# Optimization experiments

Measured on AMD Instinct MI355X. Metric: run time of the kernel, lower is better.

The kernel has to match this reference:

```python
import jax, jax.numpy as jnp
import numpy as np
from jax.ops import segment_sum, segment_max

N, E, G = 20000, 100000, 16
TILE, EMB, HID, OUT, FEAT, HEADS = 32, 128, 256, 512, 512, 8
SLOPE = 0.2


def setup_inputs() -> dict:
    key = jax.random.key(0)
    ks = jax.random.split(key, 20)
    def gn(k, shape, fan_in):
        return jax.random.normal(k, shape, jnp.float32) * (1.0 / np.sqrt(fan_in))
    return {
        "x": jax.random.normal(ks[0], (N, TILE), jnp.float32),
        "edge_index": jax.random.randint(ks[1], (2, E), 0, N, jnp.int32),
        "batch": jnp.sort(jax.random.randint(ks[2], (N,), 0, G, jnp.int32)),
        "W0": gn(ks[3], (TILE, EMB), TILE), "b0": jnp.zeros((EMB,), jnp.float32),
        "W1": gn(ks[4], (EMB, HEADS * HID), EMB),
        "a1s": gn(ks[5], (HEADS, HID), HID), "a1d": gn(ks[6], (HEADS, HID), HID),
        "b1": jnp.zeros((HEADS * HID,), jnp.float32),
        "W2": gn(ks[7], (HEADS * HID, HEADS * HID), HEADS * HID),
        "a2s": gn(ks[8], (HEADS, HID), HID), "a2d": gn(ks[9], (HEADS, HID), HID),
        "b2": jnp.zeros((HEADS * HID,), jnp.float32),
        "W3": gn(ks[10], (HEADS * HID, OUT), HEADS * HID),
        "a3s": gn(ks[11], (1, OUT), OUT), "a3d": gn(ks[12], (1, OUT), OUT),
        "b3": jnp.zeros((OUT,), jnp.float32),
        "Wf": gn(ks[13], (OUT, FEAT), OUT), "bf": jnp.zeros((FEAT,), jnp.float32),
    }


def gat_conv(x, src, dst, W, a_s, a_d, b, heads, ch, n):
    # PyG GATConv: linear, per-edge additive attention, segment softmax over dst, scatter-add
    h = (x @ W).reshape(n, heads, ch)                       # [N,H,C]
    e_src = jnp.einsum("nhc,hc->nh", h, a_s)                 # [N,H]
    e_dst = jnp.einsum("nhc,hc->nh", h, a_d)
    e = jax.nn.leaky_relu(e_src[src] + e_dst[dst], SLOPE)    # [E,H]
    m = segment_max(e, dst, num_segments=n)                  # [N,H]
    m = jax.lax.stop_gradient(jnp.where(jnp.isfinite(m), m, 0.0))
    ex = jnp.exp(e - m[dst])
    den = segment_sum(ex, dst, num_segments=n)
    alpha = ex / (den[dst] + 1e-16)                          # [E,H]
    out = segment_sum(h[src] * alpha[..., None], dst, num_segments=n)  # [N,H,C]
    return out.reshape(n, heads * ch) + b


def reference(x, edge_index, batch, W0, b0, W1, a1s, a1d, b1, W2, a2s, a2d, b2,
              W3, a3s, a3d, b3, Wf, bf):
    loop = jnp.arange(N, dtype=edge_index.dtype)             # PyG adds self-loops by default
    src = jnp.concatenate([edge_index[0], loop])
    dst = jnp.concatenate([edge_index[1], loop])
    h = jax.nn.leaky_relu(x @ W0 + b0, SLOPE)
    h = jax.nn.leaky_relu(gat_conv(h, src, dst, W1, a1s, a1d, b1, HEADS, HID, N), SLOPE)
    h = jax.nn.leaky_relu(gat_conv(h, src, dst, W2, a2s, a2d, b2, HEADS, HID, N), SLOPE)
    h = jax.nn.leaky_relu(gat_conv(h, src, dst, W3, a3s, a3d, b3, 1, OUT, N), SLOPE)
    sums = segment_sum(h, batch, num_segments=G)             # global_mean_pool
    cnt = segment_sum(jnp.ones((N,), h.dtype), batch, num_segments=G)
    mean = sums / jnp.maximum(cnt, 1.0)[:, None]
    return jax.nn.leaky_relu(mean @ Wf + bf, SLOPE)
```

## Files before the change

### kernel.cpp

```cpp
#include <hip/hip_runtime.h>
#include <hip/hip_bf16.h>

#define N_NODES 20000
#define N_EDGES 100000
#define ET (N_EDGES + N_NODES)
#define G_GRAPHS 16
#define SLOPE 0.2f

using short8  = __attribute__((ext_vector_type(8))) short;
using floatx4 = __attribute__((ext_vector_type(4))) float;

__device__ __forceinline__ float lrelu(float x) { return x > 0.f ? x : SLOPE * x; }

__device__ __forceinline__ float b2f(unsigned short u) {
    union { unsigned int i; float f; } v; v.i = ((unsigned int)u) << 16; return v.f;
}
__device__ __forceinline__ unsigned short f2b(float f) {
    union { float f; unsigned int i; } v; v.f = f;
    unsigned int i = v.i;
    return (unsigned short)((i + 0x7fffu + ((i >> 16) & 1u)) >> 16);
}

__device__ __forceinline__ void gld16(const void* g, void* l) {
    __builtin_amdgcn_global_load_lds((const __attribute__((address_space(1))) void*)g,
                                     (__attribute__((address_space(3))) void*)l, 16, 0, 0);
}

__device__ int dev_lower_bound(const int* a, int n, int key) {
    int lo = 0, hi = n;
    while (lo < hi) { int mid = (lo + hi) >> 1; if (a[mid] < key) lo = mid + 1; else hi = mid; }
    return lo;
}

__global__ void zero_kernel(int* __restrict__ p, int n) {
    int i = blockIdx.x * blockDim.x + threadIdx.x;
    if (i < n) p[i] = 0;
}

__global__ void count_kernel(const int* __restrict__ ei, int* __restrict__ counts) {
    int e = blockIdx.x * blockDim.x + threadIdx.x;
    if (e >= ET) return;
    int dst = (e < N_EDGES) ? ei[N_EDGES + e] : (e - N_EDGES);
    atomicAdd(&counts[dst], 1);
}

__global__ void scan_kernel(const int* __restrict__ counts, int* __restrict__ row_ptr) {
    __shared__ int sums[256];
    int t = threadIdx.x;
    const int CH = (N_NODES + 255) / 256;
    int base = t * CH;
    int s = 0;
    for (int i = 0; i < CH; i++) { int idx = base + i; if (idx < N_NODES) s += counts[idx]; }
    sums[t] = s;
    __syncthreads();
    for (int off = 1; off < 256; off <<= 1) {
        int v = (t >= off) ? sums[t - off] : 0;
        __syncthreads();
        sums[t] += v;
        __syncthreads();
    }
    int run = (t == 0) ? 0 : sums[t - 1];
    for (int i = 0; i < CH; i++) {
        int idx = base + i;
        if (idx < N_NODES) { row_ptr[idx] = run; run += counts[idx]; }
    }
    if (t == 255) row_ptr[N_NODES] = run;
}

__global__ void fill_kernel(const int* __restrict__ ei, const int* __restrict__ row_ptr,
                            int* __restrict__ fill_cnt, int* __restrict__ col) {
    int e = blockIdx.x * blockDim.x + threadIdx.x;
    if (e >= ET) return;
    int src, dst;
    if (e < N_EDGES) { src = ei[e]; dst = ei[N_EDGES + e]; }
    else             { src = dst = e - N_EDGES; }
    int pos = atomicAdd(&fill_cnt[dst], 1);
    col[row_ptr[dst] + pos] = src;
}

__global__ void transpose_kernel(const float* __restrict__ W, unsigned short* __restrict__ Wt,
                                 int K, int N) {
    __shared__ float tile[32][33];
    int bn = blockIdx.x * 32, bk = blockIdx.y * 32;
    int tx = threadIdx.x & 31, ty = threadIdx.x >> 5;
#pragma unroll
    for (int p = 0; p < 32; p += 8)
        tile[ty + p][tx] = W[(size_t)(bk + ty + p) * N + bn + tx];
    __syncthreads();
#pragma unroll
    for (int p = 0; p < 32; p += 8)
        Wt[(size_t)(bn + ty + p) * K + bk + tx] = f2b(tile[tx][ty + p]);
}

__global__ void gemm0_kernel(const float* __restrict__ x, const float* __restrict__ W0,
                             const float* __restrict__ b0, unsigned short* __restrict__ h0) {
    __shared__ float xr[32];
    int n = blockIdx.x, t = threadIdx.x;
    if (t < 32) xr[t] = x[n * 32 + t];
    __syncthreads();
    float acc = 0.f;
#pragma unroll
    for (int k = 0; k < 32; k++) acc += xr[k] * W0[k * 128 + t];
    h0[(size_t)n * 128 + t] = f2b(lrelu(acc + b0[t]));
}

__global__ __launch_bounds__(256) void gemm_mfma(const unsigned short* __restrict__ A,
                                                 const unsigned short* __restrict__ Bt,
                                                 unsigned short* __restrict__ C,
                                                 int M, int N, int K) {
    __shared__ __align__(16) unsigned short As[128][32];
    __shared__ __align__(16) unsigned short Bs[128][32];
    int t = threadIdx.x;
    int w = t >> 6, l = t & 63;
    int r0 = blockIdx.y * 128, c0 = blockIdx.x * 128;
    int wr = (w >> 1) * 64, wc = (w & 1) * 64;
    int lrow = l >> 2;
    int gcb  = (l & 3) ^ ((l >> 3) & 3);
    int m16 = l & 15, qb = l >> 4;
    int sw  = (m16 >> 1) & 3;
    int roff = ((qb ^ sw) * 8);
    floatx4 acc[4][4] = {};

    for (int k0 = 0; k0 < K; k0 += 32) {
        __syncthreads();
#pragma unroll
        for (int q = 0; q < 2; q++) {
            int row = w * 32 + q * 16 + lrow;
            int ga = min(r0 + row, M - 1);
            gld16(A + (size_t)ga * K + k0 + gcb * 8, &As[w * 32 + q * 16][0]);
            gld16(Bt + (size_t)(c0 + row) * K + k0 + gcb * 8, &Bs[w * 32 + q * 16][0]);
        }
        __syncthreads();
        short8 af[4], bfr[4];
#pragma unroll
        for (int i = 0; i < 4; i++) af[i] = *(const short8*)&As[wr + i * 16 + m16][roff];
#pragma unroll
        for (int j = 0; j < 4; j++) bfr[j] = *(const short8*)&Bs[wc + j * 16 + m16][roff];
#pragma unroll
        for (int i = 0; i < 4; i++)
#pragma unroll
            for (int j = 0; j < 4; j++)
                acc[i][j] = __builtin_amdgcn_mfma_f32_16x16x32_bf16(bfr[j], af[i], acc[i][j], 0, 0, 0);
    }
    int quad = l >> 4;
#pragma unroll
    for (int i = 0; i < 4; i++) {
        int r = r0 + wr + i * 16 + m16;
        if (r < M) {
#pragma unroll
            for (int j = 0; j < 4; j++) {
                int c = c0 + wc + j * 16 + quad * 4;
                ushort4 o = make_ushort4(f2b(acc[i][j][0]), f2b(acc[i][j][1]),
                                         f2b(acc[i][j][2]), f2b(acc[i][j][3]));
                *(ushort4*)&C[(size_t)r * N + c] = o;
            }
        }
    }
}

__global__ void att8_kernel(const unsigned short* __restrict__ h, const float* __restrict__ a_s,
                            const float* __restrict__ a_d, float* __restrict__ es,
                            float* __restrict__ ed) {
    int n = blockIdx.x, t = threadIdx.x;
    int hd = t >> 5, l = t & 31;
    const unsigned short* hr = h + (size_t)n * 2048 + hd * 256 + l * 8;
    const float* as_ = a_s + hd * 256 + l * 8;
    const float* ad_ = a_d + hd * 256 + l * 8;
    uint4 u = *(const uint4*)hr;
    float v[8] = { b2f((unsigned short)(u.x & 0xffff)), b2f((unsigned short)(u.x >> 16)),
                   b2f((unsigned short)(u.y & 0xffff)), b2f((unsigned short)(u.y >> 16)),
                   b2f((unsigned short)(u.z & 0xffff)), b2f((unsigned short)(u.z >> 16)),
                   b2f((unsigned short)(u.w & 0xffff)), b2f((unsigned short)(u.w >> 16)) };
    float s1 = 0.f, s2 = 0.f;
#pragma unroll
    for (int j = 0; j < 8; j++) { s1 += v[j] * as_[j]; s2 += v[j] * ad_[j]; }
    for (int m = 16; m >= 1; m >>= 1) { s1 += __shfl_xor(s1, m); s2 += __shfl_xor(s2, m); }
    if (l == 0) { es[n * 8 + hd] = s1; ed[n * 8 + hd] = s2; }
}

__global__ void att1_kernel(const unsigned short* __restrict__ h, const float* __restrict__ a_s,
                            const float* __restrict__ a_d, float* __restrict__ es,
                            float* __restrict__ ed) {
    int n = blockIdx.x, l = threadIdx.x;
    const unsigned short* hr = h + (size_t)n * 512 + l * 8;
    const float* as_ = a_s + l * 8;
    const float* ad_ = a_d + l * 8;
    uint4 u = *(const uint4*)hr;
    float v[8] = { b2f((unsigned short)(u.x & 0xffff)), b2f((unsigned short)(u.x >> 16)),
                   b2f((unsigned short)(u.y & 0xffff)), b2f((unsigned short)(u.y >> 16)),
                   b2f((unsigned short)(u.z & 0xffff)), b2f((unsigned short)(u.z >> 16)),
                   b2f((unsigned short)(u.w & 0xffff)), b2f((unsigned short)(u.w >> 16)) };
    float s1 = 0.f, s2 = 0.f;
#pragma unroll
    for (int j = 0; j < 8; j++) { s1 += v[j] * as_[j]; s2 += v[j] * ad_[j]; }
    for (int m = 32; m >= 1; m >>= 1) { s1 += __shfl_xor(s1, m); s2 += __shfl_xor(s2, m); }
    if (l == 0) { es[n] = s1; ed[n] = s2; }
}

template <int H, int C>
__global__ __launch_bounds__(256) void agg_fused(const unsigned short* __restrict__ hmid,
                                                 const float* __restrict__ es,
                                                 const float* __restrict__ ed,
                                                 const int* __restrict__ row_ptr,
                                                 const int* __restrict__ col,
                                                 const float* __restrict__ bias,
                                                 unsigned short* __restrict__ out) {
    constexpr int HC = H * C;
    constexpr int PT = HC / 256;
    int v = blockIdx.x, t = threadIdx.x;
    int rs = row_ptr[v], deg = row_ptr[v + 1] - rs;
    int j0 = t * PT;
    int hd = j0 / C;
    float edv = ed[v * H + hd];
    float acc[PT] = {};
    float den = 0.f;
    int sN = (deg > 0) ? col[rs] : 0;
    for (int e = 0; e < deg; e++) {
        int s = sN;
        if (e + 1 < deg) sN = col[rs + e + 1];
        float a = __expf(lrelu(es[s * H + hd] + edv));
        den += a;
        const unsigned short* hr = hmid + (size_t)s * HC + j0;
        if constexpr (PT == 8) {
            uint4 u = *(const uint4*)hr;
            acc[0] += a * b2f((unsigned short)(u.x & 0xffff));
            acc[1] += a * b2f((unsigned short)(u.x >> 16));
            acc[2] += a * b2f((unsigned short)(u.y & 0xffff));
            acc[3] += a * b2f((unsigned short)(u.y >> 16));
            acc[4] += a * b2f((unsigned short)(u.z & 0xffff));
            acc[5] += a * b2f((unsigned short)(u.z >> 16));
            acc[6] += a * b2f((unsigned short)(u.w & 0xffff));
            acc[7] += a * b2f((unsigned short)(u.w >> 16));
        } else {
            unsigned int u = *(const unsigned int*)hr;
            acc[0] += a * b2f((unsigned short)(u & 0xffff));
            acc[1] += a * b2f((unsigned short)(u >> 16));
        }
    }
    float inv = 1.f / (den + 1e-16f);
    unsigned short o[PT];
#pragma unroll
    for (int i = 0; i < PT; i++) o[i] = f2b(lrelu(acc[i] * inv + bias[j0 + i]));
    if constexpr (PT == 8) {
        *(uint4*)&out[(size_t)v * HC + j0] = *(const uint4*)o;
    } else {
        *(unsigned int*)&out[(size_t)v * HC + j0] = *(const unsigned int*)o;
    }
}

__global__ void pool_kernel(const unsigned short* __restrict__ h3, const int* __restrict__ batch,
                            float* __restrict__ msum) {
    int b0 = blockIdx.x * 128, t = threadIdx.x;
    int nend = min(b0 + 128, N_NODES);
    int curg = batch[b0];
    float s0 = 0.f, s1 = 0.f;
    for (int n = b0; n < nend; n++) {
        int g = batch[n];
        if (g != curg) {
            atomicAdd(&msum[curg * 512 + t * 2], s0);
            atomicAdd(&msum[curg * 512 + t * 2 + 1], s1);
            s0 = s1 = 0.f; curg = g;
        }
        unsigned int u = *(const unsigned int*)&h3[(size_t)n * 512 + t * 2];
        s0 += b2f((unsigned short)(u & 0xffff));
        s1 += b2f((unsigned short)(u >> 16));
    }
    atomicAdd(&msum[curg * 512 + t * 2], s0);
    atomicAdd(&msum[curg * 512 + t * 2 + 1], s1);
}

__global__ void final_kernel(const float* __restrict__ msum, const int* __restrict__ batch,
                             const float* __restrict__ Wf, const float* __restrict__ bf,
                             float* __restrict__ out) {
    int g = blockIdx.x, t = threadIdx.x;
    __shared__ float mr[512];
    __shared__ float sinv;
    if (t == 0) {
        int st = dev_lower_bound(batch, N_NODES, g);
        int en = dev_lower_bound(batch, N_NODES, g + 1);
        sinv = 1.f / fmaxf((float)(en - st), 1.f);
    }
    __syncthreads();
    for (int c = t; c < 512; c += 256) mr[c] = msum[g * 512 + c] * sinv;
    __syncthreads();
    for (int j = t; j < 512; j += 256) {
        float s = 0.f;
        for (int k = 0; k < 512; k++) s += mr[k] * Wf[k * 512 + j];
        out[g * 512 + j] = lrelu(s + bf[j]);
    }
}

extern "C" void kernel_launch(void* const* d_in, const int* in_sizes, int n_in,
                              void* d_out, int out_size, void* d_ws, size_t ws_size,
                              hipStream_t stream) {
    const float* x   = (const float*)d_in[0];
    const int*   ei  = (const int*)d_in[1];
    const int*   bat = (const int*)d_in[2];
    const float* W0  = (const float*)d_in[3];
    const float* b0  = (const float*)d_in[4];
    const float* W1  = (const float*)d_in[5];
    const float* a1s = (const float*)d_in[6];
    const float* a1d = (const float*)d_in[7];
    const float* b1  = (const float*)d_in[8];
    const float* W2  = (const float*)d_in[9];
    const float* a2s = (const float*)d_in[10];
    const float* a2d = (const float*)d_in[11];
    const float* b2  = (const float*)d_in[12];
    const float* W3  = (const float*)d_in[13];
    const float* a3s = (const float*)d_in[14];
    const float* a3d = (const float*)d_in[15];
    const float* b3  = (const float*)d_in[16];
    const float* Wf  = (const float*)d_in[17];
    const float* bf  = (const float*)d_in[18];
    float* out = (float*)d_out;

    char* p = (char*)d_ws;
    unsigned short* bufA = (unsigned short*)p; p += (size_t)N_NODES * 2048 * 2;
    unsigned short* bufB = (unsigned short*)p; p += (size_t)N_NODES * 2048 * 2;
    unsigned short* h0   = (unsigned short*)p; p += (size_t)N_NODES * 128 * 2;
    unsigned short* W1t  = (unsigned short*)p; p += (size_t)2048 * 128 * 2;
    unsigned short* W2t  = (unsigned short*)p; p += (size_t)2048 * 2048 * 2;
    unsigned short* W3t  = (unsigned short*)p; p += (size_t)512 * 2048 * 2;
    float* es   = (float*)p; p += (size_t)N_NODES * 8 * 4;
    float* ed   = (float*)p; p += (size_t)N_NODES * 8 * 4;
    float* msum = (float*)p; p += 16 * 512 * 4;
    int* counts  = (int*)p; p += (size_t)N_NODES * 4;
    int* row_ptr = (int*)p; p += (size_t)(N_NODES + 1) * 4;
    int* col     = (int*)p; p += (size_t)ET * 4;

    zero_kernel<<<(N_NODES + 255) / 256, 256, 0, stream>>>(counts, N_NODES);
    count_kernel<<<(ET + 255) / 256, 256, 0, stream>>>(ei, counts);
    scan_kernel<<<1, 256, 0, stream>>>(counts, row_ptr);
    zero_kernel<<<(N_NODES + 255) / 256, 256, 0, stream>>>(counts, N_NODES);
    fill_kernel<<<(ET + 255) / 256, 256, 0, stream>>>(ei, row_ptr, counts, col);

    transpose_kernel<<<dim3(2048 / 32, 128 / 32), 256, 0, stream>>>(W1, W1t, 128, 2048);
    transpose_kernel<<<dim3(2048 / 32, 2048 / 32), 256, 0, stream>>>(W2, W2t, 2048, 2048);
    transpose_kernel<<<dim3(512 / 32, 2048 / 32), 256, 0, stream>>>(W3, W3t, 2048, 512);

    gemm0_kernel<<<N_NODES, 128, 0, stream>>>(x, W0, b0, h0);

    dim3 g12(2048 / 128, (N_NODES + 127) / 128);
    dim3 g3(512 / 128, (N_NODES + 127) / 128);

    gemm_mfma<<<g12, 256, 0, stream>>>(h0, W1t, bufB, N_NODES, 2048, 128);
    att8_kernel<<<N_NODES, 256, 0, stream>>>(bufB, a1s, a1d, es, ed);
    agg_fused<8, 256><<<N_NODES, 256, 0, stream>>>(bufB, es, ed, row_ptr, col, b1, bufA);

    gemm_mfma<<<g12, 256, 0, stream>>>(bufA, W2t, bufB, N_NODES, 2048, 2048);
    att8_kernel<<<N_NODES, 256, 0, stream>>>(bufB, a2s, a2d, es, ed);
    agg_fused<8, 256><<<N_NODES, 256, 0, stream>>>(bufB, es, ed, row_ptr, col, b2, bufA);

    gemm_mfma<<<g3, 256, 0, stream>>>(bufA, W3t, bufB, N_NODES, 512, 2048);
    att1_kernel<<<N_NODES, 64, 0, stream>>>(bufB, a3s, a3d, es, ed);
    agg_fused<1, 512><<<N_NODES, 256, 0, stream>>>(bufB, es, ed, row_ptr, col, b3, bufA);

    zero_kernel<<<(16 * 512 + 255) / 256, 256, 0, stream>>>((int*)msum, 16 * 512);
    pool_kernel<<<(N_NODES + 127) / 128, 256, 0, stream>>>(bufA, bat, msum);
    final_kernel<<<G_GRAPHS, 256, 0, stream>>>(msum, bat, Wf, bf, out);
}
```

Measured before the change: 827.7 us.

## Fuse attention-score dot products into GEMM epilogue and use wave-per-node aggregation

The attention logits (h·a_src, h·a_dst) are now computed in the MFMA GEMM epilogue from fp32 accumulators, reduced across lanes and accumulated with atomics into zeroed per-layer buffers. This removes the separate att8/att1 kernels and their re-read of the bf16 feature matrix. Aggregation switches from one 256-thread block per node to one 64-lane wave per node, with each lane handling several 512-column chunks. The change adds atomics and a single larger zeroing pass, and the logits now come from unrounded fp32 values rather than bf16-rounded ones.

```diff
diff --git a/kernel.cpp b/kernel.cpp
--- a/kernel.cpp
+++ b/kernel.cpp
@@ -107,7 +107,12 @@
 __global__ __launch_bounds__(256) void gemm_mfma(const unsigned short* __restrict__ A,
                                                  const unsigned short* __restrict__ Bt,
                                                  unsigned short* __restrict__ C,
-                                                 int M, int N, int K) {
+                                                 int M, int N, int K,
+                                                 const float* __restrict__ a_s,
+                                                 const float* __restrict__ a_d,
+                                                 float* __restrict__ es,
+                                                 float* __restrict__ ed,
+                                                 int H, int head_ch) {
     __shared__ __align__(16) unsigned short As[128][32];
     __shared__ __align__(16) unsigned short Bs[128][32];
     int t = threadIdx.x;
@@ -156,95 +161,92 @@
             }
         }
     }
-}
-
-__global__ void att8_kernel(const unsigned short* __restrict__ h, const float* __restrict__ a_s,
-                            const float* __restrict__ a_d, float* __restrict__ es,
-                            float* __restrict__ ed) {
-    int n = blockIdx.x, t = threadIdx.x;
-    int hd = t >> 5, l = t & 31;
-    const unsigned short* hr = h + (size_t)n * 2048 + hd * 256 + l * 8;
-    const float* as_ = a_s + hd * 256 + l * 8;
-    const float* ad_ = a_d + hd * 256 + l * 8;
-    uint4 u = *(const uint4*)hr;
-    float v[8] = { b2f((unsigned short)(u.x & 0xffff)), b2f((unsigned short)(u.x >> 16)),
-                   b2f((unsigned short)(u.y & 0xffff)), b2f((unsigned short)(u.y >> 16)),
-                   b2f((unsigned short)(u.z & 0xffff)), b2f((unsigned short)(u.z >> 16)),
-                   b2f((unsigned short)(u.w & 0xffff)), b2f((unsigned short)(u.w >> 16)) };
-    float s1 = 0.f, s2 = 0.f;
-#pragma unroll
-    for (int j = 0; j < 8; j++) { s1 += v[j] * as_[j]; s2 += v[j] * ad_[j]; }
-    for (int m = 16; m >= 1; m >>= 1) { s1 += __shfl_xor(s1, m); s2 += __shfl_xor(s2, m); }
-    if (l == 0) { es[n * 8 + hd] = s1; ed[n * 8 + hd] = s2; }
-}
-
-__global__ void att1_kernel(const unsigned short* __restrict__ h, const float* __restrict__ a_s,
-                            const float* __restrict__ a_d, float* __restrict__ es,
-                            float* __restrict__ ed) {
-    int n = blockIdx.x, l = threadIdx.x;
-    const unsigned short* hr = h + (size_t)n * 512 + l * 8;
-    const float* as_ = a_s + l * 8;
-    const float* ad_ = a_d + l * 8;
-    uint4 u = *(const uint4*)hr;
-    float v[8] = { b2f((unsigned short)(u.x & 0xffff)), b2f((unsigned short)(u.x >> 16)),
-                   b2f((unsigned short)(u.y & 0xffff)), b2f((unsigned short)(u.y >> 16)),
-                   b2f((unsigned short)(u.z & 0xffff)), b2f((unsigned short)(u.z >> 16)),
-                   b2f((unsigned short)(u.w & 0xffff)), b2f((unsigned short)(u.w >> 16)) };
-    float s1 = 0.f, s2 = 0.f;
-#pragma unroll
-    for (int j = 0; j < 8; j++) { s1 += v[j] * as_[j]; s2 += v[j] * ad_[j]; }
-    for (int m = 32; m >= 1; m >>= 1) { s1 += __shfl_xor(s1, m); s2 += __shfl_xor(s2, m); }
-    if (l == 0) { es[n] = s1; ed[n] = s2; }
+    int base = c0 + wc;
+    int hd = base / head_ch;
+    int boff = base - hd * head_ch;
+    const float* asr = a_s + hd * head_ch + boff;
+    const float* adr = a_d + hd * head_ch + boff;
+#pragma unroll
+    for (int i = 0; i < 4; i++) {
+        int r = r0 + wr + i * 16 + m16;
+        float s1 = 0.f, s2 = 0.f;
+#pragma unroll
+        for (int j = 0; j < 4; j++)
+#pragma unroll
+            for (int reg = 0; reg < 4; reg++) {
+                int cc = j * 16 + quad * 4 + reg;
+                float av = acc[i][j][reg];
+                s1 += av * asr[cc];
+                s2 += av * adr[cc];
+            }
+        s1 += __shfl_xor(s1, 16); s2 += __shfl_xor(s2, 16);
+        s1 += __shfl_xor(s1, 32); s2 += __shfl_xor(s2, 32);
+        if (quad == 0 && r < M) {
+            atomicAdd(&es[r * H + hd], s1);
+            atomicAdd(&ed[r * H + hd], s2);
+        }
+    }
 }
 
 template <int H, int C>
-__global__ __launch_bounds__(256) void agg_fused(const unsigned short* __restrict__ hmid,
-                                                 const float* __restrict__ es,
-                                                 const float* __restrict__ ed,
-                                                 const int* __restrict__ row_ptr,
-                                                 const int* __restrict__ col,
-                                                 const float* __restrict__ bias,
-                                                 unsigned short* __restrict__ out) {
+__global__ __launch_bounds__(256) void agg_wave(const unsigned short* __restrict__ hmid,
+                                                const float* __restrict__ es,
+                                                const float* __restrict__ ed,
+                                                const int* __restrict__ row_ptr,
+                                                const int* __restrict__ col,
+                                                const float* __restrict__ bias,
+                                                unsigned short* __restrict__ out) {
     constexpr int HC = H * C;
-    constexpr int PT = HC / 256;
-    int v = blockIdx.x, t = threadIdx.x;
+    constexpr int CH = HC / 512;
+    int wv = threadIdx.x >> 6, l = threadIdx.x & 63;
+    int v = blockIdx.x * 4 + wv;
+    if (v >= N_NODES) return;
     int rs = row_ptr[v], deg = row_ptr[v + 1] - rs;
-    int j0 = t * PT;
-    int hd = j0 / C;
-    float edv = ed[v * H + hd];
-    float acc[PT] = {};
-    float den = 0.f;
+    int hd[CH];
+    float edv[CH], den[CH], acc[CH][8];
+#pragma unroll
+    for (int c = 0; c < CH; c++) {
+        hd[c] = (c * 512 + l * 8) / C;
+        edv[c] = ed[v * H + hd[c]];
+        den[c] = 0.f;
+#pragma unroll
+        for (int k = 0; k < 8; k++) acc[c][k] = 0.f;
+    }
     int sN = (deg > 0) ? col[rs] : 0;
     for (int e = 0; e < deg; e++) {
         int s = sN;
         if (e + 1 < deg) sN = col[rs + e + 1];
-        float a = __expf(lrelu(es[s * H + hd] + edv));
-        den += a;
-        const unsigned short* hr = hmid + (size_t)s * HC + j0;
-        if constexpr (PT == 8) {
-            uint4 u = *(const uint4*)hr;
-            acc[0] += a * b2f((unsigned short)(u.x & 0xffff));
-            acc[1] += a * b2f((unsigned short)(u.x >> 16));
-            acc[2] += a * b2f((unsigned short)(u.y & 0xffff));
-            acc[3] += a * b2f((unsigned short)(u.y >> 16));
-            acc[4] += a * b2f((unsigned short)(u.z & 0xffff));
-            acc[5] += a * b2f((unsigned short)(u.z >> 16));
-            acc[6] += a * b2f((unsigned short)(u.w & 0xffff));
-            acc[7] += a * b2f((unsigned short)(u.w >> 16));
-        } else {
-            unsigned int u = *(const unsigned int*)hr;
-            acc[0] += a * b2f((unsigned short)(u & 0xffff));
-            acc[1] += a * b2f((unsigned short)(u >> 16));
-        }
-    }
-    float inv = 1.f / (den + 1e-16f);
-    unsigned short o[PT];
-#pragma unroll
-    for (int i = 0; i < PT; i++) o[i] = f2b(lrelu(acc[i] * inv + bias[j0 + i]));
-    if constexpr (PT == 8) {
-        *(uint4*)&out[(size_t)v * HC + j0] = *(const uint4*)o;
-    } else {
-        *(unsigned int*)&out[(size_t)v * HC + j0] = *(const unsigned int*)o;
+        const unsigned short* hr = hmid + (size_t)s * HC + l * 8;
+        uint4 u[CH];
+#pragma unroll
+        for (int c = 0; c < CH; c++) u[c] = *(const uint4*)(hr + c * 512);
+        float ex[CH];
+#pragma unroll
+        for (int c = 0; c < CH; c++) {
+            ex[c] = __expf(lrelu(es[s * H + hd[c]] + edv[c]));
+            den[c] += ex[c];
+        }
+#pragma unroll
+        for (int c = 0; c < CH; c++) {
+            float a = ex[c];
+            acc[c][0] += a * b2f((unsigned short)(u[c].x & 0xffff));
+            acc[c][1] += a * b2f((unsigned short)(u[c].x >> 16));
+            acc[c][2] += a * b2f((unsigned short)(u[c].y & 0xffff));
+            acc[c][3] += a * b2f((unsigned short)(u[c].y >> 16));
+            acc[c][4] += a * b2f((unsigned short)(u[c].z & 0xffff));
+            acc[c][5] += a * b2f((unsigned short)(u[c].z >> 16));
+            acc[c][6] += a * b2f((unsigned short)(u[c].w & 0xffff));
+            acc[c][7] += a * b2f((unsigned short)(u[c].w >> 16));
+        }
+    }
+#pragma unroll
+    for (int c = 0; c < CH; c++) {
+        float inv = 1.f / (den[c] + 1e-16f);
+        unsigned short o[8];
+#pragma unroll
+        for (int k = 0; k < 8; k++)
+            o[k] = f2b(lrelu(acc[c][k] * inv + bias[c * 512 + l * 8 + k]));
+        *(uint4*)&out[(size_t)v * HC + c * 512 + l * 8] = *(const uint4*)o;
     }
 }
 
@@ -321,9 +323,15 @@
     unsigned short* W1t  = (unsigned short*)p; p += (size_t)2048 * 128 * 2;
     unsigned short* W2t  = (unsigned short*)p; p += (size_t)2048 * 2048 * 2;
     unsigned short* W3t  = (unsigned short*)p; p += (size_t)512 * 2048 * 2;
-    float* es   = (float*)p; p += (size_t)N_NODES * 8 * 4;
-    float* ed   = (float*)p; p += (size_t)N_NODES * 8 * 4;
+    float* zreg = (float*)p;
+    float* es1 = (float*)p; p += (size_t)N_NODES * 8 * 4;
+    float* ed1 = (float*)p; p += (size_t)N_NODES * 8 * 4;
+    float* es2 = (float*)p; p += (size_t)N_NODES * 8 * 4;
+    float* ed2 = (float*)p; p += (size_t)N_NODES * 8 * 4;
+    float* es3 = (float*)p; p += (size_t)N_NODES * 4;
+    float* ed3 = (float*)p; p += (size_t)N_NODES * 4;
     float* msum = (float*)p; p += 16 * 512 * 4;
+    const int ZN = N_NODES * 8 * 4 + N_NODES * 2 + 16 * 512;
     int* counts  = (int*)p; p += (size_t)N_NODES * 4;
     int* row_ptr = (int*)p; p += (size_t)(N_NODES + 1) * 4;
     int* col     = (int*)p; p += (size_t)ET * 4;
@@ -338,24 +346,26 @@
     transpose_kernel<<<dim3(2048 / 32, 2048 / 32), 256, 0, stream>>>(W2, W2t, 2048, 2048);
     transpose_kernel<<<dim3(512 / 32, 2048 / 32), 256, 0, stream>>>(W3, W3t, 2048, 512);
 
+    zero_kernel<<<(ZN + 255) / 256, 256, 0, stream>>>((int*)zreg, ZN);
+
     gemm0_kernel<<<N_NODES, 128, 0, stream>>>(x, W0, b0, h0);
 
     dim3 g12(2048 / 128, (N_NODES + 127) / 128);
     dim3 g3(512 / 128, (N_NODES + 127) / 128);
-
-    gemm_mfma<<<g12, 256, 0, stream>>>(h0, W1t, bufB, N_NODES, 2048, 128);
-    att8_kernel<<<N_NODES, 256, 0, stream>>>(bufB, a1s, a1d, es, ed);
-    agg_fused<8, 256><<<N_NODES, 256, 0, stream>>>(bufB, es, ed, row_ptr, col, b1, bufA);
-
-    gemm_mfma<<<g12, 256, 0, stream>>>(bufA, W2t, bufB, N_NODES, 2048, 2048);
-    att8_kernel<<<N_NODES, 256, 0, stream>>>(bufB, a2s, a2d, es, ed);
-    agg_fused<8, 256><<<N_NODES, 256, 0, stream>>>(bufB, es, ed, row_ptr, col, b2, bufA);
-
-    gemm_mfma<<<g3, 256, 0, stream>>>(bufA, W3t, bufB, N_NODES, 512, 2048);
-    att1_kernel<<<N_NODES, 64, 0, stream>>>(bufB, a3s, a3d, es, ed);
-    agg_fused<1, 512><<<N_NODES, 256, 0, stream>>>(bufB, es, ed, row_ptr, col, b3, bufA);
-
-    zero_kernel<<<(16 * 512 + 255) / 256, 256, 0, stream>>>((int*)msum, 16 * 512);
+    int aggb = (N_NODES + 3) / 4;
+
+    gemm_mfma<<<g12, 256, 0, stream>>>(h0, W1t, bufB, N_NODES, 2048, 128,
+                                       a1s, a1d, es1, ed1, 8, 256);
+    agg_wave<8, 256><<<aggb, 256, 0, stream>>>(bufB, es1, ed1, row_ptr, col, b1, bufA);
+
+    gemm_mfma<<<g12, 256, 0, stream>>>(bufA, W2t, bufB, N_NODES, 2048, 2048,
+                                       a2s, a2d, es2, ed2, 8, 256);
+    agg_wave<8, 256><<<aggb, 256, 0, stream>>>(bufB, es2, ed2, row_ptr, col, b2, bufA);
+
+    gemm_mfma<<<g3, 256, 0, stream>>>(bufA, W3t, bufB, N_NODES, 512, 2048,
+                                      a3s, a3d, es3, ed3, 1, 512);
+    agg_wave<1, 512><<<aggb, 256, 0, stream>>>(bufB, es3, ed3, row_ptr, col, b3, bufA);
+
     pool_kernel<<<(N_NODES + 127) / 128, 256, 0, stream>>>(bufA, bat, msum);
     final_kernel<<<G_GRAPHS, 256, 0, stream>>>(msum, bat, Wf, bf, out);
 }
```

Result: slower. 881.4 us (+6.5%).
